# Optimization experiments

Measured on AMD Instinct MI355X. Metric: run time of the kernel, lower is better.

## Reference

```python
import jax, jax.numpy as jnp
import numpy as np

B = 128        # graphs per side
NPG = 512      # nodes per graph (equal-sized for jit)
N = B * NPG    # 65536 total nodes
E = 1048576    # edges per side
IN = 128       # input feature dim
H = 64         # hidden dim
BINS = 16      # histogram bins over [-1, 1]


def setup_inputs() -> dict:
    key = jax.random.key(0)
    ks = jax.random.split(key, 20)
    inp = {}
    inp["x1"] = jax.random.normal(ks[0], (N, IN), jnp.float32)
    inp["e1"] = jax.random.randint(ks[1], (2, E), 0, N)
    inp["b1"] = jnp.arange(N, dtype=jnp.int32) // NPG
    inp["x2"] = jax.random.normal(ks[2], (N, IN), jnp.float32)
    inp["e2"] = jax.random.randint(ks[3], (2, E), 0, N)
    inp["b2"] = jnp.arange(N, dtype=jnp.int32) // NPG
    def lin(k, fi, fo):
        s = 1.0 / np.sqrt(fi)
        return jax.random.uniform(k, (fi, fo), jnp.float32, -s, s)
    # GIN encoder (shared across both graph sides): conv1 MLP, conv2 MLP
    inp["enc_w1"] = lin(ks[4], IN, H); inp["enc_b1"] = jnp.zeros((H,), jnp.float32)
    inp["enc_w2"] = lin(ks[5], H, H);  inp["enc_b2"] = jnp.zeros((H,), jnp.float32)
    inp["enc_w3"] = lin(ks[6], H, H);  inp["enc_b3"] = jnp.zeros((H,), jnp.float32)
    inp["enc_w4"] = lin(ks[7], H, H);  inp["enc_b4"] = jnp.zeros((H,), jnp.float32)
    # final MLP: (2H + BINS + 3) -> H -> H//2 -> 1
    FIN = 2 * H + BINS + 3
    inp["mlp_w1"] = lin(ks[8], FIN, H);      inp["mlp_b1"] = jnp.zeros((H,), jnp.float32)
    inp["mlp_w2"] = lin(ks[9], H, H // 2);   inp["mlp_b2"] = jnp.zeros((H // 2,), jnp.float32)
    inp["mlp_w3"] = lin(ks[10], H // 2, 1);  inp["mlp_b3"] = jnp.zeros((1,), jnp.float32)
    return inp


def _gin_layer(x, src, dst, wa, ba, wb, bb):
    # GINConv (eps=0): mlp(x + sum_{j->i} x_j), then encoder-level ReLU
    agg = jax.ops.segment_sum(x[src], dst, num_segments=N)
    h = x + agg
    h = jnp.maximum(h @ wa + ba, 0.0) @ wb + bb
    return jnp.maximum(h, 0.0)


def _encode(x, e, enc_w1, enc_b1, enc_w2, enc_b2, enc_w3, enc_b3, enc_w4, enc_b4):
    src, dst = e[0], e[1]
    h = _gin_layer(x, src, dst, enc_w1, enc_b1, enc_w2, enc_b2)
    h = _gin_layer(h, src, dst, enc_w3, enc_b3, enc_w4, enc_b4)
    return h


def _hist_stats(h1, h2):
    # h1, h2: [N, H] node embeddings; equal-sized graphs -> [B, NPG, H]
    E1 = h1.reshape(B, NPG, H)
    E2 = h2.reshape(B, NPG, H)
    E1n = E1 / jnp.maximum(jnp.linalg.norm(E1, axis=-1, keepdims=True), 1e-12)
    E2n = E2 / jnp.maximum(jnp.linalg.norm(E2, axis=-1, keepdims=True), 1e-12)
    sim = jnp.einsum('bnd,bmd->bnm', E1n, E2n)          # [B, NPG, NPG]
    flat = sim.reshape(B, NPG * NPG)
    # histc over [-1, 1] with BINS bins (right-edge values go to last bin)
    idx = jnp.clip(jnp.floor((flat + 1.0) * (BINS / 2.0)), 0, BINS - 1).astype(jnp.int32)
    seg = (jnp.arange(B, dtype=jnp.int32)[:, None] * BINS + idx).reshape(-1)
    hist = jax.ops.segment_sum(jnp.ones((B * NPG * NPG,), jnp.float32), seg,
                               num_segments=B * BINS).reshape(B, BINS)
    hist = hist / jnp.maximum(hist.sum(axis=1, keepdims=True), 1.0)
    stats = jnp.stack([flat.mean(axis=1), flat.max(axis=1), flat.std(axis=1)], axis=1)
    return jnp.concatenate([hist, stats], axis=1)        # [B, BINS+3]


def reference(x1, e1, b1, x2, e2, b2,
              enc_w1, enc_b1, enc_w2, enc_b2, enc_w3, enc_b3, enc_w4, enc_b4,
              mlp_w1, mlp_b1, mlp_w2, mlp_b2, mlp_w3, mlp_b3):
    h1 = _encode(x1, e1, enc_w1, enc_b1, enc_w2, enc_b2, enc_w3, enc_b3, enc_w4, enc_b4)
    h2 = _encode(x2, e2, enc_w1, enc_b1, enc_w2, enc_b2, enc_w3, enc_b3, enc_w4, enc_b4)
    # global_mean_pool: equal-sized contiguous graphs -> reshape mean
    g1 = h1.reshape(B, NPG, H).mean(axis=1)
    g2 = h2.reshape(B, NPG, H).mean(axis=1)
    sim_feats = _hist_stats(h1, h2)
    f = jnp.concatenate([g1, g2, sim_feats], axis=1)     # [B, 2H+BINS+3]
    f = jnp.maximum(f @ mlp_w1 + mlp_b1, 0.0)            # dropout = identity (eval)
    f = jnp.maximum(f @ mlp_w2 + mlp_b2, 0.0)
    out = (f @ mlp_w3 + mlp_b3)[:, 0]                    # [B]
    return out
```

## Files before the change

### kernel.cpp

```cpp
#include <hip/hip_runtime.h>
#include <hip/hip_bf16.h>
#include <hip/hip_fp16.h>

namespace {

constexpr int N    = 65536;
constexpr int E    = 1048576;
constexpr int N2   = 2 * N;
constexpr int B    = 128;
constexpr int NPG  = 512;
constexpr int IN   = 128;
constexpr int H    = 64;
constexpr int BINS = 16;
constexpr int FIN  = 2 * H + BINS + 3;
constexpr int NBUCKET = 512;
constexpr int NSLICE  = 512;
constexpr int SLICE_E = 4096;

typedef _Float16 f16x8 __attribute__((ext_vector_type(8)));
typedef float f32x16 __attribute__((ext_vector_type(16)));

union FragU { f16x8 v; unsigned int u[4]; };

__device__ __forceinline__ unsigned packh(float a, float b) {
  typedef __fp16 fp16x2 __attribute__((ext_vector_type(2)));
  union { fp16x2 h; unsigned u; } t;
  t.h = __builtin_amdgcn_cvt_pkrtz(a, b);
  return t.u;
}

__device__ __forceinline__ f16x8 ldf16x8(const __half* p) {
  return *(const f16x8*)(const void*)p;
}


__global__ __launch_bounds__(256) void k_p1_xw(const int* __restrict__ dst1, const int* __restrict__ dst2,
                                               int* __restrict__ bcnt,
                                               const float* __restrict__ x1, const float* __restrict__ x2,
                                               const float* __restrict__ W, __half* __restrict__ y,
                                               const float* __restrict__ Wa, const float* __restrict__ Wb,
                                               const float* __restrict__ Wc, __half* __restrict__ WaT,
                                               __half* __restrict__ WbT, __half* __restrict__ WcT) {
  __shared__ int hist[NBUCKET];
  int b = blockIdx.x, tid = threadIdx.x;
  if (b < NSLICE) {
    hist[tid] = 0;
    hist[tid + 256] = 0;
    __syncthreads();
    const int* d = (b < 256) ? dst1 : dst2;
    int ebase = (b & 255) * SLICE_E;
    int boff = (b < 256) ? 0 : 256;
    for (int i = tid; i < SLICE_E; i += 256) atomicAdd(&hist[boff + (d[ebase + i] >> 8)], 1);
    __syncthreads();
    for (int k = tid; k < NBUCKET; k += 256) bcnt[b * NBUCKET + k] = hist[k];
  } else if (b < NSLICE + N2 / 128) {
    int wv = tid >> 6, lane = tid & 63;
    int nodebase = ((b - NSLICE) * 4 + wv) * 32;
    const float* xp = (nodebase < N) ? (x1 + (size_t)nodebase * IN)
                                     : (x2 + (size_t)(nodebase - N) * IN);
    int r = lane & 31;
    int kh = lane >> 5;
    const float* xrow = xp + (size_t)r * IN + kh * 8;
    f32x16 acc0, acc1;
#pragma unroll
    for (int i = 0; i < 16; ++i) { acc0[i] = 0.f; acc1[i] = 0.f; }
#pragma unroll
    for (int kk = 0; kk < 8; ++kk) {
      float4 a0 = *(const float4*)(xrow + kk * 16);
      float4 a1 = *(const float4*)(xrow + kk * 16 + 4);
      f16x8 af;
      af[0] = (_Float16)a0.x; af[1] = (_Float16)a0.y; af[2] = (_Float16)a0.z; af[3] = (_Float16)a0.w;
      af[4] = (_Float16)a1.x; af[5] = (_Float16)a1.y; af[6] = (_Float16)a1.z; af[7] = (_Float16)a1.w;
      const float* wbase = W + (size_t)(kk * 16 + kh * 8) * H + r;
      f16x8 b0, b1;
#pragma unroll
      for (int j = 0; j < 8; ++j) {
        b0[j] = (_Float16)wbase[j * H];
        b1[j] = (_Float16)wbase[j * H + 32];
      }
      acc0 = __builtin_amdgcn_mfma_f32_32x32x16_f16(af, b0, acc0, 0, 0, 0);
      acc1 = __builtin_amdgcn_mfma_f32_32x32x16_f16(af, b1, acc1, 0, 0, 0);
    }
#pragma unroll
    for (int reg = 0; reg < 16; ++reg) {
      int row = (reg & 3) + 8 * (reg >> 2) + 4 * kh;
      y[(size_t)(nodebase + row) * H + r]      = __float2half(acc0[reg]);
      y[(size_t)(nodebase + row) * H + r + 32] = __float2half(acc1[reg]);
    }
  } else {
    int i = (b - NSLICE - N2 / 128) * 256 + tid;
    int k = i >> 6, h = i & 63;
    WaT[h * 64 + k] = __float2half(Wa[k * 64 + h]);
    WbT[h * 64 + k] = __float2half(Wb[k * 64 + h]);
    WcT[h * 64 + k] = __float2half(Wc[k * 64 + h]);
  }
}

__global__ __launch_bounds__(256) void k_scanrows(const int* __restrict__ bcnt, int* __restrict__ boffs,
                                                  int* __restrict__ tot) {
  __shared__ int s[NSLICE];
  int b = blockIdx.x, t = threadIdx.x;
  int v0 = bcnt[t * NBUCKET + b], v1 = bcnt[(t + 256) * NBUCKET + b];
  s[t] = v0;
  s[t + 256] = v1;
  __syncthreads();
  for (int d = 1; d < NSLICE; d <<= 1) {
    int a0 = (t >= d) ? s[t - d] : 0;
    int a1 = (t + 256 >= d) ? s[t + 256 - d] : 0;
    __syncthreads();
    s[t] += a0;
    s[t + 256] += a1;
    __syncthreads();
  }
  boffs[b * NSLICE + t] = s[t] - v0;
  boffs[b * NSLICE + t + 256] = s[t + 256] - v1;
  if (t == 255) tot[b] = s[NSLICE - 1];
}

__global__ __launch_bounds__(256) void k_p5(const int* __restrict__ src1, const int* __restrict__ dst1,
                                            const int* __restrict__ src2, const int* __restrict__ dst2,
                                            const int* __restrict__ boffs, const int* __restrict__ tot,
                                            int* __restrict__ ebuf) {
  __shared__ int stot[NBUCKET];
  __shared__ int sofs[NBUCKET];
  __shared__ int cur[NBUCKET];
  int b = blockIdx.x, tid = threadIdx.x;
  int v0 = tot[tid], v1 = tot[tid + 256];
  stot[tid] = v0;
  stot[tid + 256] = v1;
  __syncthreads();
  for (int d = 1; d < NBUCKET; d <<= 1) {
    int a0 = (tid >= d) ? stot[tid - d] : 0;
    int a1 = (tid + 256 >= d) ? stot[tid + 256 - d] : 0;
    __syncthreads();
    stot[tid] += a0;
    stot[tid + 256] += a1;
    __syncthreads();
  }
  sofs[tid]       = stot[tid] - v0 + boffs[tid * NSLICE + b];
  sofs[tid + 256] = stot[tid + 256] - v1 + boffs[(tid + 256) * NSLICE + b];
  cur[tid] = 0;
  cur[tid + 256] = 0;
  __syncthreads();
  const int* sr = (b < 256) ? src1 : src2;
  const int* d  = (b < 256) ? dst1 : dst2;
  int ebase = (b & 255) * SLICE_E;
  int off = (b < 256) ? 0 : N;
  int boff2 = (b < 256) ? 0 : 256;
  for (int i = tid; i < SLICE_E; i += 256) {
    int dd = d[ebase + i];
    int sv = off + sr[ebase + i];
    int bucket = boff2 + (dd >> 8);
    int r = atomicAdd(&cur[bucket], 1);
    ebuf[sofs[bucket] + r] = ((dd & 255) << 17) | sv;
  }
}

__global__ __launch_bounds__(256) void k_p6(const int* __restrict__ ebuf, const int* __restrict__ tot,
                                            int* __restrict__ rowptr, int* __restrict__ col) {
  __shared__ int stot[NBUCKET];
  __shared__ int c256[256];
  __shared__ int lofs[256];
  int b = blockIdx.x, t = threadIdx.x;
  {
    int v0 = tot[t], v1 = tot[t + 256];
    stot[t] = v0;
    stot[t + 256] = v1;
    __syncthreads();
    for (int d = 1; d < NBUCKET; d <<= 1) {
      int a0 = (t >= d) ? stot[t - d] : 0;
      int a1 = (t + 256 >= d) ? stot[t + 256 - d] : 0;
      __syncthreads();
      stot[t] += a0;
      stot[t + 256] += a1;
      __syncthreads();
    }
  }
  int e0 = (b == 0) ? 0 : stot[b - 1];
  int e1 = stot[b];
  c256[t] = 0;
  __syncthreads();
  for (int i = e0 + t; i < e1; i += 256) atomicAdd(&c256[(ebuf[i] >> 17) & 255], 1);
  __syncthreads();
  int v = c256[t];
  lofs[t] = v;
  __syncthreads();
  for (int d = 1; d < 256; d <<= 1) {
    int a = (t >= d) ? lofs[t - d] : 0;
    __syncthreads();
    lofs[t] += a;
    __syncthreads();
  }
  int excl = lofs[t] - v;
  rowptr[b * 256 + t] = e0 + excl;
  if (b == 0 && t == 0) rowptr[N2] = 2 * E;
  c256[t] = 0;
  lofs[t] = excl;
  __syncthreads();
  for (int i = e0 + t; i < e1; i += 256) {
    int pk = ebuf[i];
    int dl = (pk >> 17) & 255;
    int r = atomicAdd(&c256[dl], 1);
    col[e0 + lofs[dl] + r] = pk & 0x1FFFF;
  }
}


__global__ __launch_bounds__(256) void k_gather(const __half* __restrict__ in, const int* __restrict__ rowptr,
                                                const int* __restrict__ col, const float* __restrict__ bias,
                                                __half* __restrict__ outb) {
  int tid = threadIdx.x;
  int lane32 = tid & 31;
  int n = blockIdx.x * 8 + (tid >> 5);
  const __half2* in2 = (const __half2*)in;
  __half2* out2 = (__half2*)outb;
  float2 bias2 = ((const float2*)bias)[lane32];
  int p0 = rowptr[n], p1 = rowptr[n + 1];
  int deg = p1 - p0;
  int pc = (p1 - 1 > p0) ? p1 - 1 : p0;
  int cidx = p0 + lane32;
  int c0 = col[cidx < pc ? cidx : pc];
  __half2 self = in2[(size_t)n * 32 + lane32];
  float ax = __half2float(self.x) + bias2.x;
  float ay = __half2float(self.y) + bias2.y;
  float cx = 0.f, cy = 0.f;
  if (deg > 0) {
    __half2 vl;
    {
      __half2 v[16];
#pragma unroll
      for (int i = 0; i < 16; ++i) {
        int c = __shfl(c0, i, 32);
        v[i] = in2[(size_t)c * 32 + lane32];
      }
#pragma unroll
      for (int i = 0; i < 16; i += 4) {
        __half2 w0 = __hadd2(v[i], v[i + 1]);
        __half2 w1 = __hadd2(v[i + 2], v[i + 3]);
        ax += __half2float(w0.x);
        ay += __half2float(w0.y);
        cx += __half2float(w1.x);
        cy += __half2float(w1.y);
      }
      vl = v[15];
    }
    if (deg > 16) {
      __half2 v[16];
#pragma unroll
      for (int i = 0; i < 16; ++i) {
        int c = __shfl(c0, i + 16, 32);
        v[i] = in2[(size_t)c * 32 + lane32];
      }
#pragma unroll
      for (int i = 0; i < 16; i += 4) {
        __half2 w0 = __hadd2(v[i], v[i + 1]);
        __half2 w1 = __hadd2(v[i + 2], v[i + 3]);
        ax += __half2float(w0.x);
        ay += __half2float(w0.y);
        cx += __half2float(w1.x);
        cy += __half2float(w1.y);
      }
      vl = v[15];
    }
    if (deg > 32) {
      for (int p = p0 + 32; p < p1; ++p) {
        int c = col[p];
        __half2 v = in2[(size_t)c * 32 + lane32];
        ax += __half2float(v.x);
        ay += __half2float(v.y);
      }
    }
    int cov = (deg > 16) ? 32 : 16;
    int dup = cov - (deg < cov ? deg : cov);
    float fd = (float)dup;
    ax -= fd * __half2float(vl.x);
    ay -= fd * __half2float(vl.y);
  }
  __half2 o;
  o.x = __float2half(fmaxf(ax + cx, 0.f));
  o.y = __float2half(fmaxf(ay + cy, 0.f));
  out2[(size_t)n * 32 + lane32] = o;
}

__global__ __launch_bounds__(256) void k_mid(const __half* __restrict__ in, const __half* __restrict__ WaT,
                                             const float* __restrict__ ba, const __half* __restrict__ WbT,
                                             __half* __restrict__ outb) {
  int tid = threadIdx.x, wv = tid >> 6, lane = tid & 63;
  int nodebase = (blockIdx.x * 4 + wv) * 32;
  int r = lane & 31, kh = lane >> 5;
  f32x16 acc0, acc1;
#pragma unroll
  for (int i = 0; i < 16; ++i) { acc0[i] = 0.f; acc1[i] = 0.f; }
  const __half* brow = in + (size_t)(nodebase + r) * H + kh * 8;
#pragma unroll
  for (int kk = 0; kk < 4; ++kk) {
    f16x8 bf = ldf16x8(brow + kk * 16);
    f16x8 a0 = ldf16x8(WaT + (size_t)r * H + kk * 16 + kh * 8);
    f16x8 a1 = ldf16x8(WaT + (size_t)(r + 32) * H + kk * 16 + kh * 8);
    acc0 = __builtin_amdgcn_mfma_f32_32x32x16_f16(a0, bf, acc0, 0, 0, 0);
    acc1 = __builtin_amdgcn_mfma_f32_32x32x16_f16(a1, bf, acc1, 0, 0, 0);
  }
  float bav = ba[lane];
  unsigned p0[8], p1[8];
#pragma unroll
  for (int g2 = 0; g2 < 8; ++g2) {
    int regA = 2 * g2, regB = 2 * g2 + 1;
    int rowA = (regA & 3) + 8 * (regA >> 2) + 4 * kh;
    int rowB = (regB & 3) + 8 * (regB >> 2) + 4 * kh;
    float tA0 = fmaxf(acc0[regA] + __shfl(bav, rowA, 64), 0.f);
    float tB0 = fmaxf(acc0[regB] + __shfl(bav, rowB, 64), 0.f);
    float tA1 = fmaxf(acc1[regA] + __shfl(bav, rowA + 32, 64), 0.f);
    float tB1 = fmaxf(acc1[regB] + __shfl(bav, rowB + 32, 64), 0.f);
    p0[g2] = packh(tA0, tB0);
    p1[g2] = packh(tA1, tB1);
  }
  unsigned q0[8], q1[8];
#pragma unroll
  for (int i = 0; i < 8; ++i) {
    q0[i] = (unsigned)__shfl_xor((int)p0[i], 32, 64);
    q1[i] = (unsigned)__shfl_xor((int)p1[i], 32, 64);
  }
  bool hi = (kh != 0);
  f32x16 o0, o1;
#pragma unroll
  for (int i = 0; i < 16; ++i) { o0[i] = 0.f; o1[i] = 0.f; }
#pragma unroll
  for (int kk = 0; kk < 4; ++kk) {
    const unsigned* P = (kk < 2) ? p0 : p1;
    const unsigned* Q = (kk < 2) ? q0 : q1;
    int s = kk & 1;
    FragU f;
    f.u[0] = hi ? Q[4 * s + 2] : P[4 * s + 0];
    f.u[1] = hi ? Q[4 * s + 3] : P[4 * s + 1];
    f.u[2] = hi ? P[4 * s + 2] : Q[4 * s + 0];
    f.u[3] = hi ? P[4 * s + 3] : Q[4 * s + 1];
    f16x8 b0 = ldf16x8(WbT + (size_t)r * H + kk * 16 + kh * 8);
    f16x8 b1 = ldf16x8(WbT + (size_t)(r + 32) * H + kk * 16 + kh * 8);
    o0 = __builtin_amdgcn_mfma_f32_32x32x16_f16(f.v, b0, o0, 0, 0, 0);
    o1 = __builtin_amdgcn_mfma_f32_32x32x16_f16(f.v, b1, o1, 0, 0, 0);
  }
#pragma unroll
  for (int reg = 0; reg < 16; ++reg) {
    int row = (reg & 3) + 8 * (reg >> 2) + 4 * kh;
    outb[(size_t)(nodebase + row) * H + r]      = __float2half(o0[reg]);
    outb[(size_t)(nodebase + row) * H + r + 32] = __float2half(o1[reg]);
  }
}

__global__ __launch_bounds__(256) void k_last(const __half* __restrict__ in, const __half* __restrict__ WcT,
                                              const float* __restrict__ b4, __half* __restrict__ outn,
                                              float* __restrict__ pg) {
  int tid = threadIdx.x, wv = tid >> 6, lane = tid & 63;
  int tile = blockIdx.x * 4 + wv;
  int nodebase = tile * 32;
  int r = lane & 31, kh = lane >> 5;
  f32x16 acc0, acc1;
#pragma unroll
  for (int i = 0; i < 16; ++i) { acc0[i] = 0.f; acc1[i] = 0.f; }
  const __half* arow = in + (size_t)(nodebase + r) * H + kh * 8;
#pragma unroll
  for (int kk = 0; kk < 4; ++kk) {
    f16x8 af = ldf16x8(arow + kk * 16);
    f16x8 b0 = ldf16x8(WcT + (size_t)r * H + kk * 16 + kh * 8);
    f16x8 b1 = ldf16x8(WcT + (size_t)(r + 32) * H + kk * 16 + kh * 8);
    acc0 = __builtin_amdgcn_mfma_f32_32x32x16_f16(af, b0, acc0, 0, 0, 0);
    acc1 = __builtin_amdgcn_mfma_f32_32x32x16_f16(af, b1, acc1, 0, 0, 0);
  }
  float bA = b4[r], bB = b4[r + 32];
  float psum0 = 0.f, psum1 = 0.f;
#pragma unroll
  for (int reg = 0; reg < 16; ++reg) {
    int row = (reg & 3) + 8 * (reg >> 2) + 4 * kh;
    float h0 = fmaxf(acc0[reg] + bA, 0.f);
    float h1 = fmaxf(acc1[reg] + bB, 0.f);
    psum0 += h0;
    psum1 += h1;
    float ss = h0 * h0 + h1 * h1;
#pragma unroll
    for (int d = 1; d < 32; d <<= 1) ss += __shfl_xor(ss, d, 64);
    float inv = 1.f / fmaxf(sqrtf(ss), 1e-12f);
    outn[(size_t)(nodebase + row) * H + r]      = __float2half(h0 * inv);
    outn[(size_t)(nodebase + row) * H + r + 32] = __float2half(h1 * inv);
  }
  psum0 += __shfl_xor(psum0, 32, 64);
  psum1 += __shfl_xor(psum1, 32, 64);
  if (kh == 0) {
    pg[tile * 64 + r]      = psum0;
    pg[tile * 64 + r + 32] = psum1;
  }
}

__global__ __launch_bounds__(256) void k_sim(const __half* __restrict__ Hn, float* __restrict__ psum,
                                             float* __restrict__ psumsq, float* __restrict__ pmax,
                                             int* __restrict__ phist) {
  __shared__ int shist[64 * 17];
  __shared__ float sfin[4][4];
  int tid = threadIdx.x, lane = tid & 63, wv = tid >> 6;
  int g = blockIdx.x >> 3, rt = blockIdx.x & 7;
  for (int i = tid; i < 64 * 17; i += 256) shist[i] = 0;
  __syncthreads();

  int rtile = wv & 1;
  int cgrp  = wv >> 1;
  int arow = lane & 31;
  int koff = (lane >> 5) * 8;

  const __half* H1 = Hn + ((size_t)g * NPG + rt * 64 + rtile * 32 + arow) * H + koff;
  f16x8 afrag[4];
#pragma unroll
  for (int kk = 0; kk < 4; ++kk) afrag[kk] = ldf16x8(H1 + kk * 16);

  const __half* H2g = Hn + ((size_t)N + (size_t)g * NPG + arow) * H + koff;
  float lmax = -2.f, lsum = 0.f, lsumsq = 0.f;
  int rep = lane * 17;
#pragma unroll 1
  for (int t = 0; t < 8; ++t) {
    int ct = cgrp * 8 + t;
    const __half* B0 = H2g + (size_t)(ct * 32) * H;
    f32x16 acc;
#pragma unroll
    for (int r = 0; r < 16; ++r) acc[r] = 0.f;
#pragma unroll
    for (int kk = 0; kk < 4; ++kk) {
      f16x8 bfrag = ldf16x8(B0 + kk * 16);
      acc = __builtin_amdgcn_mfma_f32_32x32x16_f16(afrag[kk], bfrag, acc, 0, 0, 0);
    }
#pragma unroll
    for (int r = 0; r < 16; ++r) {
      float v = acc[r];
      lmax = fmaxf(lmax, v);
      lsum += v;
      lsumsq = fmaf(v, v, lsumsq);
      int bin = (int)((v + 1.f) * 8.f);
      bin = bin < 0 ? 0 : (bin > BINS - 1 ? BINS - 1 : bin);
      atomicAdd(&shist[rep + bin], 1);
    }
  }
#pragma unroll
  for (int d = 1; d < 64; d <<= 1) {
    lsum += __shfl_xor(lsum, d, 64);
    lsumsq += __shfl_xor(lsumsq, d, 64);
    lmax = fmaxf(lmax, __shfl_xor(lmax, d, 64));
  }
  if (lane == 0) {
    sfin[wv][0] = lsum;
    sfin[wv][1] = lsumsq;
    sfin[wv][2] = lmax;
  }
  __syncthreads();
  if (tid == 0) {
    psum[blockIdx.x] = sfin[0][0] + sfin[1][0] + sfin[2][0] + sfin[3][0];
    psumsq[blockIdx.x] = sfin[0][1] + sfin[1][1] + sfin[2][1] + sfin[3][1];
    pmax[blockIdx.x] = fmaxf(fmaxf(sfin[0][2], sfin[1][2]), fmaxf(sfin[2][2], sfin[3][2]));
  }
  if (tid < BINS) {
    int tot = 0;
    for (int r = 0; r < 64; ++r) tot += shist[r * 17 + tid];
    phist[blockIdx.x * BINS + tid] = tot;
  }
}

__global__ __launch_bounds__(64) void k_final(const float* __restrict__ pg1, const float* __restrict__ pg2,
                                              const float* __restrict__ psum, const float* __restrict__ psumsq,
                                              const float* __restrict__ pmax, const int* __restrict__ phist,
                                              const float* __restrict__ w1, const float* __restrict__ b1,
                                              const float* __restrict__ w2, const float* __restrict__ b2,
                                              const float* __restrict__ w3, const float* __restrict__ b3,
                                              float* __restrict__ out) {
  __shared__ float f[FIN + 1];
  __shared__ float t1[64];
  __shared__ float t2[32];
  int g = blockIdx.x, t = threadIdx.x;
  {
    float s1v = 0.f, s2v = 0.f;
#pragma unroll
    for (int r = 0; r < 16; ++r) {
      s1v += pg1[(g * 16 + r) * 64 + t];
      s2v += pg2[(g * 16 + r) * 64 + t];
    }
    f[t]      = s1v * (1.f / NPG);
    f[64 + t] = s2v * (1.f / NPG);
  }
  if (t < BINS) {
    int tot = 0;
#pragma unroll
    for (int r = 0; r < 8; ++r) tot += phist[(g * 8 + r) * BINS + t];
    f[2 * H + t] = (float)tot * (1.f / 262144.f);
  }
  if (t == 0) {
    float s = 0.f, ss = 0.f, mx = -2.f;
#pragma unroll
    for (int r = 0; r < 8; ++r) {
      s += psum[g * 8 + r];
      ss += psumsq[g * 8 + r];
      mx = fmaxf(mx, pmax[g * 8 + r]);
    }
    const float inv = 1.f / 262144.f;
    float mean = s * inv;
    float var = fmaxf(ss * inv - mean * mean, 0.f);
    f[144] = mean;
    f[145] = mx;
    f[146] = sqrtf(var);
  }
  __syncthreads();
  float acc = b1[t];
  for (int k = 0; k < FIN; ++k) acc = fmaf(f[k], w1[k * 64 + t], acc);
  t1[t] = fmaxf(acc, 0.f);
  __syncthreads();
  if (t < 32) {
    float a2 = b2[t];
#pragma unroll 8
    for (int k = 0; k < 64; ++k) a2 = fmaf(t1[k], w2[k * 32 + t], a2);
    t2[t] = fmaxf(a2, 0.f);
  }
  __syncthreads();
  if (t == 0) {
    float a3 = b3[0];
#pragma unroll
    for (int k = 0; k < 32; ++k) a3 = fmaf(t2[k], w3[k], a3);
    out[g] = a3;
  }
}

}

extern "C" void kernel_launch(void* const* d_in, const int* in_sizes, int n_in, void* d_out, int out_size,
                              void* d_ws, size_t ws_size, hipStream_t stream) {
  const float* x1 = (const float*)d_in[0];
  const int* e1 = (const int*)d_in[1];
  const float* x2 = (const float*)d_in[3];
  const int* e2 = (const int*)d_in[4];
  const float* enc_w1 = (const float*)d_in[6];
  const float* enc_b1 = (const float*)d_in[7];
  const float* enc_w2 = (const float*)d_in[8];
  const float* enc_b2 = (const float*)d_in[9];
  const float* enc_w3 = (const float*)d_in[10];
  const float* enc_b3 = (const float*)d_in[11];
  const float* enc_w4 = (const float*)d_in[12];
  const float* enc_b4 = (const float*)d_in[13];
  const float* mw1 = (const float*)d_in[14];
  const float* mb1 = (const float*)d_in[15];
  const float* mw2 = (const float*)d_in[16];
  const float* mb2 = (const float*)d_in[17];
  const float* mw3 = (const float*)d_in[18];
  const float* mb3 = (const float*)d_in[19];
  float* out = (float*)d_out;

  char* wsc = (char*)d_ws;
  size_t off = 0;
  auto alloc = [&](size_t bytes) -> void* {
    void* p = wsc + off;
    off += (bytes + 255) & ~(size_t)255;
    return p;
  };
  __half* Hn = (__half*)alloc((size_t)N2 * H * 2);
  __half* yH = (__half*)alloc((size_t)N2 * H * 2);
  __half* tH = (__half*)alloc((size_t)N2 * H * 2);
  __half* zH = (__half*)alloc((size_t)N2 * H * 2);
  __half* t2H = (__half*)alloc((size_t)N2 * H * 2);
  int* rowptr = (int*)alloc((size_t)(N2 + 1) * 4);
  int* colidx = (int*)alloc((size_t)2 * E * 4);
  int* bcnt = (int*)alloc((size_t)NSLICE * NBUCKET * 4);
  int* boffs = (int*)alloc((size_t)NBUCKET * NSLICE * 4);
  int* tot = (int*)alloc((size_t)NBUCKET * 4);
  float* pg = (float*)alloc((size_t)(N2 / 32) * 64 * 4);
  float* psum = (float*)alloc(1024 * 4);
  float* psumsq = (float*)alloc(1024 * 4);
  float* pmaxa = (float*)alloc(1024 * 4);
  int* phist = (int*)alloc((size_t)1024 * BINS * 4);
  __half* WaT = (__half*)alloc(4096 * 2);
  __half* WbT = (__half*)alloc(4096 * 2);
  __half* WcT = (__half*)alloc(4096 * 2);
  (void)ws_size;
  (void)in_sizes;
  (void)n_in;
  (void)out_size;

  const int* src1 = e1;
  const int* dst1 = e1 + E;
  const int* src2 = e2;
  const int* dst2 = e2 + E;
  int* ebuf = (int*)tH;

  k_p1_xw<<<NSLICE + N2 / 128 + 16, 256, 0, stream>>>(dst1, dst2, bcnt, x1, x2, enc_w1, yH,
                                                      enc_w2, enc_w3, enc_w4, WaT, WbT, WcT);
  k_scanrows<<<NBUCKET, 256, 0, stream>>>(bcnt, boffs, tot);
  k_p5<<<NSLICE, 256, 0, stream>>>(src1, dst1, src2, dst2, boffs, tot, ebuf);
  k_p6<<<NBUCKET, 256, 0, stream>>>(ebuf, tot, rowptr, colidx);

  k_gather<<<N2 / 8, 256, 0, stream>>>(yH, rowptr, colidx, enc_b1, tH);
  k_mid<<<N2 / 128, 256, 0, stream>>>(tH, WaT, enc_b2, WbT, zH);
  k_gather<<<N2 / 8, 256, 0, stream>>>(zH, rowptr, colidx, enc_b3, t2H);
  k_last<<<N2 / 128, 256, 0, stream>>>(t2H, WcT, enc_b4, Hn, pg);

  k_sim<<<B * 8, 256, 0, stream>>>(Hn, psum, psumsq, pmaxa, phist);
  k_final<<<B, 64, 0, stream>>>(pg, pg + (size_t)2048 * 64, psum, psumsq, pmaxa, phist, mw1, mb1, mw2, mb2,
                                mw3, mb3, out);
}
```

Baseline: 185.6 us.

## Fuse neighbor gather into MLP kernels via padded LDS tiles

The standalone gather kernels are folded into the MFMA kernels. Each wavefront gathers its 32 nodes (two nodes per round, 32 lanes each) into a padded shared-memory tile, then runs the MFMA matmul from LDS. This removes the round-trip of the aggregated tensors through global memory and two kernel launches. The cost is lower parallelism during the gather phase, since each wave now loops over 16 rounds of latency-bound neighbor loads with fewer resident waves.

```diff
diff --git a/kernel.cpp b/kernel.cpp
--- a/kernel.cpp
+++ b/kernel.cpp
@@ -16,6 +16,7 @@
 constexpr int NBUCKET = 512;
 constexpr int NSLICE  = 512;
 constexpr int SLICE_E = 4096;
+constexpr int TPAD = 72;
 
 typedef _Float16 f16x8 __attribute__((ext_vector_type(8)));
 typedef float f32x16 __attribute__((ext_vector_type(16)));
@@ -33,188 +34,10 @@
   return *(const f16x8*)(const void*)p;
 }
 
-
-__global__ __launch_bounds__(256) void k_p1_xw(const int* __restrict__ dst1, const int* __restrict__ dst2,
-                                               int* __restrict__ bcnt,
-                                               const float* __restrict__ x1, const float* __restrict__ x2,
-                                               const float* __restrict__ W, __half* __restrict__ y,
-                                               const float* __restrict__ Wa, const float* __restrict__ Wb,
-                                               const float* __restrict__ Wc, __half* __restrict__ WaT,
-                                               __half* __restrict__ WbT, __half* __restrict__ WcT) {
-  __shared__ int hist[NBUCKET];
-  int b = blockIdx.x, tid = threadIdx.x;
-  if (b < NSLICE) {
-    hist[tid] = 0;
-    hist[tid + 256] = 0;
-    __syncthreads();
-    const int* d = (b < 256) ? dst1 : dst2;
-    int ebase = (b & 255) * SLICE_E;
-    int boff = (b < 256) ? 0 : 256;
-    for (int i = tid; i < SLICE_E; i += 256) atomicAdd(&hist[boff + (d[ebase + i] >> 8)], 1);
-    __syncthreads();
-    for (int k = tid; k < NBUCKET; k += 256) bcnt[b * NBUCKET + k] = hist[k];
-  } else if (b < NSLICE + N2 / 128) {
-    int wv = tid >> 6, lane = tid & 63;
-    int nodebase = ((b - NSLICE) * 4 + wv) * 32;
-    const float* xp = (nodebase < N) ? (x1 + (size_t)nodebase * IN)
-                                     : (x2 + (size_t)(nodebase - N) * IN);
-    int r = lane & 31;
-    int kh = lane >> 5;
-    const float* xrow = xp + (size_t)r * IN + kh * 8;
-    f32x16 acc0, acc1;
-#pragma unroll
-    for (int i = 0; i < 16; ++i) { acc0[i] = 0.f; acc1[i] = 0.f; }
-#pragma unroll
-    for (int kk = 0; kk < 8; ++kk) {
-      float4 a0 = *(const float4*)(xrow + kk * 16);
-      float4 a1 = *(const float4*)(xrow + kk * 16 + 4);
-      f16x8 af;
-      af[0] = (_Float16)a0.x; af[1] = (_Float16)a0.y; af[2] = (_Float16)a0.z; af[3] = (_Float16)a0.w;
-      af[4] = (_Float16)a1.x; af[5] = (_Float16)a1.y; af[6] = (_Float16)a1.z; af[7] = (_Float16)a1.w;
-      const float* wbase = W + (size_t)(kk * 16 + kh * 8) * H + r;
-      f16x8 b0, b1;
-#pragma unroll
-      for (int j = 0; j < 8; ++j) {
-        b0[j] = (_Float16)wbase[j * H];
-        b1[j] = (_Float16)wbase[j * H + 32];
-      }
-      acc0 = __builtin_amdgcn_mfma_f32_32x32x16_f16(af, b0, acc0, 0, 0, 0);
-      acc1 = __builtin_amdgcn_mfma_f32_32x32x16_f16(af, b1, acc1, 0, 0, 0);
-    }
-#pragma unroll
-    for (int reg = 0; reg < 16; ++reg) {
-      int row = (reg & 3) + 8 * (reg >> 2) + 4 * kh;
-      y[(size_t)(nodebase + row) * H + r]      = __float2half(acc0[reg]);
-      y[(size_t)(nodebase + row) * H + r + 32] = __float2half(acc1[reg]);
-    }
-  } else {
-    int i = (b - NSLICE - N2 / 128) * 256 + tid;
-    int k = i >> 6, h = i & 63;
-    WaT[h * 64 + k] = __float2half(Wa[k * 64 + h]);
-    WbT[h * 64 + k] = __float2half(Wb[k * 64 + h]);
-    WcT[h * 64 + k] = __float2half(Wc[k * 64 + h]);
-  }
-}
-
-__global__ __launch_bounds__(256) void k_scanrows(const int* __restrict__ bcnt, int* __restrict__ boffs,
-                                                  int* __restrict__ tot) {
-  __shared__ int s[NSLICE];
-  int b = blockIdx.x, t = threadIdx.x;
-  int v0 = bcnt[t * NBUCKET + b], v1 = bcnt[(t + 256) * NBUCKET + b];
-  s[t] = v0;
-  s[t + 256] = v1;
-  __syncthreads();
-  for (int d = 1; d < NSLICE; d <<= 1) {
-    int a0 = (t >= d) ? s[t - d] : 0;
-    int a1 = (t + 256 >= d) ? s[t + 256 - d] : 0;
-    __syncthreads();
-    s[t] += a0;
-    s[t + 256] += a1;
-    __syncthreads();
-  }
-  boffs[b * NSLICE + t] = s[t] - v0;
-  boffs[b * NSLICE + t + 256] = s[t + 256] - v1;
-  if (t == 255) tot[b] = s[NSLICE - 1];
-}
-
-__global__ __launch_bounds__(256) void k_p5(const int* __restrict__ src1, const int* __restrict__ dst1,
-                                            const int* __restrict__ src2, const int* __restrict__ dst2,
-                                            const int* __restrict__ boffs, const int* __restrict__ tot,
-                                            int* __restrict__ ebuf) {
-  __shared__ int stot[NBUCKET];
-  __shared__ int sofs[NBUCKET];
-  __shared__ int cur[NBUCKET];
-  int b = blockIdx.x, tid = threadIdx.x;
-  int v0 = tot[tid], v1 = tot[tid + 256];
-  stot[tid] = v0;
-  stot[tid + 256] = v1;
-  __syncthreads();
-  for (int d = 1; d < NBUCKET; d <<= 1) {
-    int a0 = (tid >= d) ? stot[tid - d] : 0;
-    int a1 = (tid + 256 >= d) ? stot[tid + 256 - d] : 0;
-    __syncthreads();
-    stot[tid] += a0;
-    stot[tid + 256] += a1;
-    __syncthreads();
-  }
-  sofs[tid]       = stot[tid] - v0 + boffs[tid * NSLICE + b];
-  sofs[tid + 256] = stot[tid + 256] - v1 + boffs[(tid + 256) * NSLICE + b];
-  cur[tid] = 0;
-  cur[tid + 256] = 0;
-  __syncthreads();
-  const int* sr = (b < 256) ? src1 : src2;
-  const int* d  = (b < 256) ? dst1 : dst2;
-  int ebase = (b & 255) * SLICE_E;
-  int off = (b < 256) ? 0 : N;
-  int boff2 = (b < 256) ? 0 : 256;
-  for (int i = tid; i < SLICE_E; i += 256) {
-    int dd = d[ebase + i];
-    int sv = off + sr[ebase + i];
-    int bucket = boff2 + (dd >> 8);
-    int r = atomicAdd(&cur[bucket], 1);
-    ebuf[sofs[bucket] + r] = ((dd & 255) << 17) | sv;
-  }
-}
-
-__global__ __launch_bounds__(256) void k_p6(const int* __restrict__ ebuf, const int* __restrict__ tot,
-                                            int* __restrict__ rowptr, int* __restrict__ col) {
-  __shared__ int stot[NBUCKET];
-  __shared__ int c256[256];
-  __shared__ int lofs[256];
-  int b = blockIdx.x, t = threadIdx.x;
-  {
-    int v0 = tot[t], v1 = tot[t + 256];
-    stot[t] = v0;
-    stot[t + 256] = v1;
-    __syncthreads();
-    for (int d = 1; d < NBUCKET; d <<= 1) {
-      int a0 = (t >= d) ? stot[t - d] : 0;
-      int a1 = (t + 256 >= d) ? stot[t + 256 - d] : 0;
-      __syncthreads();
-      stot[t] += a0;
-      stot[t + 256] += a1;
-      __syncthreads();
-    }
-  }
-  int e0 = (b == 0) ? 0 : stot[b - 1];
-  int e1 = stot[b];
-  c256[t] = 0;
-  __syncthreads();
-  for (int i = e0 + t; i < e1; i += 256) atomicAdd(&c256[(ebuf[i] >> 17) & 255], 1);
-  __syncthreads();
-  int v = c256[t];
-  lofs[t] = v;
-  __syncthreads();
-  for (int d = 1; d < 256; d <<= 1) {
-    int a = (t >= d) ? lofs[t - d] : 0;
-    __syncthreads();
-    lofs[t] += a;
-    __syncthreads();
-  }
-  int excl = lofs[t] - v;
-  rowptr[b * 256 + t] = e0 + excl;
-  if (b == 0 && t == 0) rowptr[N2] = 2 * E;
-  c256[t] = 0;
-  lofs[t] = excl;
-  __syncthreads();
-  for (int i = e0 + t; i < e1; i += 256) {
-    int pk = ebuf[i];
-    int dl = (pk >> 17) & 255;
-    int r = atomicAdd(&c256[dl], 1);
-    col[e0 + lofs[dl] + r] = pk & 0x1FFFF;
-  }
-}
-
-
-__global__ __launch_bounds__(256) void k_gather(const __half* __restrict__ in, const int* __restrict__ rowptr,
-                                                const int* __restrict__ col, const float* __restrict__ bias,
-                                                __half* __restrict__ outb) {
-  int tid = threadIdx.x;
-  int lane32 = tid & 31;
-  int n = blockIdx.x * 8 + (tid >> 5);
-  const __half2* in2 = (const __half2*)in;
-  __half2* out2 = (__half2*)outb;
-  float2 bias2 = ((const float2*)bias)[lane32];
+__device__ __forceinline__ __half2 gather_node2(const __half2* __restrict__ in2,
+                                                const int* __restrict__ rowptr,
+                                                const int* __restrict__ col, int n, int lane32,
+                                                float2 bias2) {
   int p0 = rowptr[n], p1 = rowptr[n + 1];
   int deg = p1 - p0;
   int pc = (p1 - 1 > p0) ? p1 - 1 : p0;
@@ -279,19 +102,202 @@
   __half2 o;
   o.x = __float2half(fmaxf(ax + cx, 0.f));
   o.y = __float2half(fmaxf(ay + cy, 0.f));
-  out2[(size_t)n * 32 + lane32] = o;
-}
-
-__global__ __launch_bounds__(256) void k_mid(const __half* __restrict__ in, const __half* __restrict__ WaT,
-                                             const float* __restrict__ ba, const __half* __restrict__ WbT,
-                                             __half* __restrict__ outb) {
+  return o;
+}
+
+
+__global__ __launch_bounds__(256) void k_p1_xw(const int* __restrict__ dst1, const int* __restrict__ dst2,
+                                               int* __restrict__ bcnt,
+                                               const float* __restrict__ x1, const float* __restrict__ x2,
+                                               const float* __restrict__ W, __half* __restrict__ y,
+                                               const float* __restrict__ Wa, const float* __restrict__ Wb,
+                                               const float* __restrict__ Wc, __half* __restrict__ WaT,
+                                               __half* __restrict__ WbT, __half* __restrict__ WcT) {
+  __shared__ int hist[NBUCKET];
+  int b = blockIdx.x, tid = threadIdx.x;
+  if (b < NSLICE) {
+    hist[tid] = 0;
+    hist[tid + 256] = 0;
+    __syncthreads();
+    const int* d = (b < 256) ? dst1 : dst2;
+    int ebase = (b & 255) * SLICE_E;
+    int boff = (b < 256) ? 0 : 256;
+    for (int i = tid; i < SLICE_E; i += 256) atomicAdd(&hist[boff + (d[ebase + i] >> 8)], 1);
+    __syncthreads();
+    for (int k = tid; k < NBUCKET; k += 256) bcnt[b * NBUCKET + k] = hist[k];
+  } else if (b < NSLICE + N2 / 128) {
+    int wv = tid >> 6, lane = tid & 63;
+    int nodebase = ((b - NSLICE) * 4 + wv) * 32;
+    const float* xp = (nodebase < N) ? (x1 + (size_t)nodebase * IN)
+                                     : (x2 + (size_t)(nodebase - N) * IN);
+    int r = lane & 31;
+    int kh = lane >> 5;
+    const float* xrow = xp + (size_t)r * IN + kh * 8;
+    f32x16 acc0, acc1;
+#pragma unroll
+    for (int i = 0; i < 16; ++i) { acc0[i] = 0.f; acc1[i] = 0.f; }
+#pragma unroll
+    for (int kk = 0; kk < 8; ++kk) {
+      float4 a0 = *(const float4*)(xrow + kk * 16);
+      float4 a1 = *(const float4*)(xrow + kk * 16 + 4);
+      f16x8 af;
+      af[0] = (_Float16)a0.x; af[1] = (_Float16)a0.y; af[2] = (_Float16)a0.z; af[3] = (_Float16)a0.w;
+      af[4] = (_Float16)a1.x; af[5] = (_Float16)a1.y; af[6] = (_Float16)a1.z; af[7] = (_Float16)a1.w;
+      const float* wbase = W + (size_t)(kk * 16 + kh * 8) * H + r;
+      f16x8 b0, b1;
+#pragma unroll
+      for (int j = 0; j < 8; ++j) {
+        b0[j] = (_Float16)wbase[j * H];
+        b1[j] = (_Float16)wbase[j * H + 32];
+      }
+      acc0 = __builtin_amdgcn_mfma_f32_32x32x16_f16(af, b0, acc0, 0, 0, 0);
+      acc1 = __builtin_amdgcn_mfma_f32_32x32x16_f16(af, b1, acc1, 0, 0, 0);
+    }
+#pragma unroll
+    for (int reg = 0; reg < 16; ++reg) {
+      int row = (reg & 3) + 8 * (reg >> 2) + 4 * kh;
+      y[(size_t)(nodebase + row) * H + r]      = __float2half(acc0[reg]);
+      y[(size_t)(nodebase + row) * H + r + 32] = __float2half(acc1[reg]);
+    }
+  } else {
+    int i = (b - NSLICE - N2 / 128) * 256 + tid;
+    int k = i >> 6, h = i & 63;
+    WaT[h * 64 + k] = __float2half(Wa[k * 64 + h]);
+    WbT[h * 64 + k] = __float2half(Wb[k * 64 + h]);
+    WcT[h * 64 + k] = __float2half(Wc[k * 64 + h]);
+  }
+}
+
+__global__ __launch_bounds__(256) void k_scanrows(const int* __restrict__ bcnt, int* __restrict__ boffs,
+                                                  int* __restrict__ tot) {
+  __shared__ int s[NSLICE];
+  int b = blockIdx.x, t = threadIdx.x;
+  int v0 = bcnt[t * NBUCKET + b], v1 = bcnt[(t + 256) * NBUCKET + b];
+  s[t] = v0;
+  s[t + 256] = v1;
+  __syncthreads();
+  for (int d = 1; d < NSLICE; d <<= 1) {
+    int a0 = (t >= d) ? s[t - d] : 0;
+    int a1 = (t + 256 >= d) ? s[t + 256 - d] : 0;
+    __syncthreads();
+    s[t] += a0;
+    s[t + 256] += a1;
+    __syncthreads();
+  }
+  boffs[b * NSLICE + t] = s[t] - v0;
+  boffs[b * NSLICE + t + 256] = s[t + 256] - v1;
+  if (t == 255) tot[b] = s[NSLICE - 1];
+}
+
+__global__ __launch_bounds__(256) void k_p5(const int* __restrict__ src1, const int* __restrict__ dst1,
+                                            const int* __restrict__ src2, const int* __restrict__ dst2,
+                                            const int* __restrict__ boffs, const int* __restrict__ tot,
+                                            int* __restrict__ ebuf) {
+  __shared__ int stot[NBUCKET];
+  __shared__ int sofs[NBUCKET];
+  __shared__ int cur[NBUCKET];
+  int b = blockIdx.x, tid = threadIdx.x;
+  int v0 = tot[tid], v1 = tot[tid + 256];
+  stot[tid] = v0;
+  stot[tid + 256] = v1;
+  __syncthreads();
+  for (int d = 1; d < NBUCKET; d <<= 1) {
+    int a0 = (tid >= d) ? stot[tid - d] : 0;
+    int a1 = (tid + 256 >= d) ? stot[tid + 256 - d] : 0;
+    __syncthreads();
+    stot[tid] += a0;
+    stot[tid + 256] += a1;
+    __syncthreads();
+  }
+  sofs[tid]       = stot[tid] - v0 + boffs[tid * NSLICE + b];
+  sofs[tid + 256] = stot[tid + 256] - v1 + boffs[(tid + 256) * NSLICE + b];
+  cur[tid] = 0;
+  cur[tid + 256] = 0;
+  __syncthreads();
+  const int* sr = (b < 256) ? src1 : src2;
+  const int* d  = (b < 256) ? dst1 : dst2;
+  int ebase = (b & 255) * SLICE_E;
+  int off = (b < 256) ? 0 : N;
+  int boff2 = (b < 256) ? 0 : 256;
+  for (int i = tid; i < SLICE_E; i += 256) {
+    int dd = d[ebase + i];
+    int sv = off + sr[ebase + i];
+    int bucket = boff2 + (dd >> 8);
+    int r = atomicAdd(&cur[bucket], 1);
+    ebuf[sofs[bucket] + r] = ((dd & 255) << 17) | sv;
+  }
+}
+
+__global__ __launch_bounds__(256) void k_p6(const int* __restrict__ ebuf, const int* __restrict__ tot,
+                                            int* __restrict__ rowptr, int* __restrict__ col) {
+  __shared__ int stot[NBUCKET];
+  __shared__ int c256[256];
+  __shared__ int lofs[256];
+  int b = blockIdx.x, t = threadIdx.x;
+  {
+    int v0 = tot[t], v1 = tot[t + 256];
+    stot[t] = v0;
+    stot[t + 256] = v1;
+    __syncthreads();
+    for (int d = 1; d < NBUCKET; d <<= 1) {
+      int a0 = (t >= d) ? stot[t - d] : 0;
+      int a1 = (t + 256 >= d) ? stot[t + 256 - d] : 0;
+      __syncthreads();
+      stot[t] += a0;
+      stot[t + 256] += a1;
+      __syncthreads();
+    }
+  }
+  int e0 = (b == 0) ? 0 : stot[b - 1];
+  int e1 = stot[b];
+  c256[t] = 0;
+  __syncthreads();
+  for (int i = e0 + t; i < e1; i += 256) atomicAdd(&c256[(ebuf[i] >> 17) & 255], 1);
+  __syncthreads();
+  int v = c256[t];
+  lofs[t] = v;
+  __syncthreads();
+  for (int d = 1; d < 256; d <<= 1) {
+    int a = (t >= d) ? lofs[t - d] : 0;
+    __syncthreads();
+    lofs[t] += a;
+    __syncthreads();
+  }
+  int excl = lofs[t] - v;
+  rowptr[b * 256 + t] = e0 + excl;
+  if (b == 0 && t == 0) rowptr[N2] = 2 * E;
+  c256[t] = 0;
+  lofs[t] = excl;
+  __syncthreads();
+  for (int i = e0 + t; i < e1; i += 256) {
+    int pk = ebuf[i];
+    int dl = (pk >> 17) & 255;
+    int r = atomicAdd(&c256[dl], 1);
+    col[e0 + lofs[dl] + r] = pk & 0x1FFFF;
+  }
+}
+
+__global__ __launch_bounds__(256) void k_gmid(const __half* __restrict__ in, const int* __restrict__ rowptr,
+                                              const int* __restrict__ col, const float* __restrict__ b0v,
+                                              const __half* __restrict__ WaT, const float* __restrict__ ba,
+                                              const __half* __restrict__ WbT, __half* __restrict__ outb) {
+  __shared__ __align__(16) __half lds_t[4][32 * TPAD];
   int tid = threadIdx.x, wv = tid >> 6, lane = tid & 63;
+  int lane32 = lane & 31, sub = lane >> 5;
   int nodebase = (blockIdx.x * 4 + wv) * 32;
-  int r = lane & 31, kh = lane >> 5;
+  const __half2* in2 = (const __half2*)in;
+  float2 bias2 = ((const float2*)b0v)[lane32];
+#pragma unroll 2
+  for (int round = 0; round < 16; ++round) {
+    int row = 2 * round + sub;
+    __half2 o = gather_node2(in2, rowptr, col, nodebase + row, lane32, bias2);
+    *(__half2*)&lds_t[wv][row * TPAD + lane32 * 2] = o;
+  }
+  int r = lane32, kh = sub;
   f32x16 acc0, acc1;
 #pragma unroll
   for (int i = 0; i < 16; ++i) { acc0[i] = 0.f; acc1[i] = 0.f; }
-  const __half* brow = in + (size_t)(nodebase + r) * H + kh * 8;
+  const __half* brow = &lds_t[wv][r * TPAD + kh * 8];
 #pragma unroll
   for (int kk = 0; kk < 4; ++kk) {
     f16x8 bf = ldf16x8(brow + kk * 16);
@@ -347,17 +353,28 @@
   }
 }
 
-__global__ __launch_bounds__(256) void k_last(const __half* __restrict__ in, const __half* __restrict__ WcT,
-                                              const float* __restrict__ b4, __half* __restrict__ outn,
-                                              float* __restrict__ pg) {
+__global__ __launch_bounds__(256) void k_glast(const __half* __restrict__ in, const int* __restrict__ rowptr,
+                                               const int* __restrict__ col, const float* __restrict__ b0v,
+                                               const __half* __restrict__ WcT, const float* __restrict__ b4,
+                                               __half* __restrict__ outn, float* __restrict__ pg) {
+  __shared__ __align__(16) __half lds_t[4][32 * TPAD];
   int tid = threadIdx.x, wv = tid >> 6, lane = tid & 63;
+  int lane32 = lane & 31, sub = lane >> 5;
   int tile = blockIdx.x * 4 + wv;
   int nodebase = tile * 32;
-  int r = lane & 31, kh = lane >> 5;
+  const __half2* in2 = (const __half2*)in;
+  float2 bias2 = ((const float2*)b0v)[lane32];
+#pragma unroll 2
+  for (int round = 0; round < 16; ++round) {
+    int row = 2 * round + sub;
+    __half2 o = gather_node2(in2, rowptr, col, nodebase + row, lane32, bias2);
+    *(__half2*)&lds_t[wv][row * TPAD + lane32 * 2] = o;
+  }
+  int r = lane32, kh = sub;
   f32x16 acc0, acc1;
 #pragma unroll
   for (int i = 0; i < 16; ++i) { acc0[i] = 0.f; acc1[i] = 0.f; }
-  const __half* arow = in + (size_t)(nodebase + r) * H + kh * 8;
+  const __half* arow = &lds_t[wv][r * TPAD + kh * 8];
 #pragma unroll
   for (int kk = 0; kk < 4; ++kk) {
     f16x8 af = ldf16x8(arow + kk * 16);
@@ -555,9 +572,7 @@
   };
   __half* Hn = (__half*)alloc((size_t)N2 * H * 2);
   __half* yH = (__half*)alloc((size_t)N2 * H * 2);
-  __half* tH = (__half*)alloc((size_t)N2 * H * 2);
   __half* zH = (__half*)alloc((size_t)N2 * H * 2);
-  __half* t2H = (__half*)alloc((size_t)N2 * H * 2);
   int* rowptr = (int*)alloc((size_t)(N2 + 1) * 4);
   int* colidx = (int*)alloc((size_t)2 * E * 4);
   int* bcnt = (int*)alloc((size_t)NSLICE * NBUCKET * 4);
@@ -580,7 +595,7 @@
   const int* dst1 = e1 + E;
   const int* src2 = e2;
   const int* dst2 = e2 + E;
-  int* ebuf = (int*)tH;
+  int* ebuf = (int*)zH;
 
   k_p1_xw<<<NSLICE + N2 / 128 + 16, 256, 0, stream>>>(dst1, dst2, bcnt, x1, x2, enc_w1, yH,
                                                       enc_w2, enc_w3, enc_w4, WaT, WbT, WcT);
@@ -588,10 +603,8 @@
   k_p5<<<NSLICE, 256, 0, stream>>>(src1, dst1, src2, dst2, boffs, tot, ebuf);
   k_p6<<<NBUCKET, 256, 0, stream>>>(ebuf, tot, rowptr, colidx);
 
-  k_gather<<<N2 / 8, 256, 0, stream>>>(yH, rowptr, colidx, enc_b1, tH);
-  k_mid<<<N2 / 128, 256, 0, stream>>>(tH, WaT, enc_b2, WbT, zH);
-  k_gather<<<N2 / 8, 256, 0, stream>>>(zH, rowptr, colidx, enc_b3, t2H);
-  k_last<<<N2 / 128, 256, 0, stream>>>(t2H, WcT, enc_b4, Hn, pg);
+  k_gmid<<<N2 / 128, 256, 0, stream>>>(yH, rowptr, colidx, enc_b1, WaT, enc_b2, WbT, zH);
+  k_glast<<<N2 / 128, 256, 0, stream>>>(zH, rowptr, colidx, enc_b3, WcT, enc_b4, Hn, pg);
 
   k_sim<<<B * 8, 256, 0, stream>>>(Hn, psum, psumsq, pmaxa, phist);
   k_final<<<B, 64, 0, stream>>>(pg, pg + (size_t)2048 * 64, psum, psumsq, pmaxa, phist, mw1, mb1, mw2, mb2,
```

Result: no change. 186.4 us (+0.5%).
